# Kernel optimization log

Measured on AMD Instinct MI355X. Metric: run time of the kernel, lower is better.

Reference implementation:

```python
import jax, jax.numpy as jnp
import numpy as np

B, N, T, N_IN = 4, 40, 64, 4
N_EMB, N_HID = 32, 64
EPS = 1e-05


def _spatial_rels(n):
    # fully-connected directed edges without self-loops (NRI convention)
    offdiag = np.ones((n, n)) - np.eye(n)
    recv_idx, send_idx = np.where(offdiag)[0], np.where(offdiag)[1]
    eye = np.eye(n, dtype=np.float32)
    return eye[recv_idx], eye[send_idx]  # [n*(n-1), n] each


def _temporal_rels(t):
    # all t*t ordered pairs (including self), one-hot
    eye = np.eye(t, dtype=np.float32)
    recv = np.repeat(np.arange(t), t)
    send = np.tile(np.arange(t), t)
    return eye[recv], eye[send]  # [t*t, t] each


def setup_inputs() -> dict:
    key = jax.random.key(0)
    ks = jax.random.split(key, 8)
    rel_rec, rel_send = _spatial_rels(N)
    rel_rec_t, rel_send_t = _temporal_rels(T)
    s_emb = 1.0 / np.sqrt(N_IN)
    s_lstm = 1.0 / np.sqrt(N_HID)
    s_att = 1.0 / np.sqrt(2 * N_HID)
    return {
        "inputs": jax.random.normal(ks[0], (B, N, T, N_IN), dtype=jnp.float32),
        "rel_rec": jnp.asarray(rel_rec),
        "rel_send": jnp.asarray(rel_send),
        "rel_rec_t": jnp.asarray(rel_rec_t),
        "rel_send_t": jnp.asarray(rel_send_t),
        "W_emb": jax.random.uniform(ks[1], (N_EMB, N_IN), jnp.float32, -s_emb, s_emb),
        "b_emb": jnp.zeros((N_EMB,), jnp.float32),
        "W_ih": jax.random.uniform(ks[2], (4 * N_HID, N_EMB), jnp.float32, -s_lstm, s_lstm),
        "W_hh": jax.random.uniform(ks[3], (4 * N_HID, N_HID), jnp.float32, -s_lstm, s_lstm),
        "b_ih": jax.random.uniform(ks[4], (4 * N_HID,), jnp.float32, -s_lstm, s_lstm),
        "b_hh": jax.random.uniform(ks[5], (4 * N_HID,), jnp.float32, -s_lstm, s_lstm),
        "W_att": jax.random.uniform(ks[6], (1, 2 * N_HID), jnp.float32, -s_att, s_att),
        "b_att": jnp.zeros((1,), jnp.float32),
    }


def _forward(inputs, rel_rec, rel_send, rel_rec_t, rel_send_t,
             W_emb, b_emb, W_ih, W_hh, b_ih, b_hh, W_att, b_att):
    b, n, t, _ = inputs.shape
    nh = W_hh.shape[1]
    locs = inputs[..., :2]

    # ---- LSTMEncoder: per-timestep embedding + LSTM cell (scan over time) ----
    emb = jnp.einsum("bnti,ei->bnte", inputs, W_emb) + b_emb       # [B,N,T,n_emb]
    xs = emb.transpose(2, 0, 1, 3).reshape(t, b * n, -1)            # [T,BN,n_emb]

    def step(carry, x):
        h, c = carry
        gates = x @ W_ih.T + b_ih + h @ W_hh.T + b_hh               # [BN,4H]
        i_g, f_g, g_g, o_g = jnp.split(gates, 4, axis=-1)           # torch gate order i,f,g,o
        i_g = jax.nn.sigmoid(i_g)
        f_g = jax.nn.sigmoid(f_g)
        g_g = jnp.tanh(g_g)
        o_g = jax.nn.sigmoid(o_g)
        c = f_g * c + i_g * g_g
        h = o_g * jnp.tanh(c)
        return (h, c), h

    h0 = jnp.zeros((b * n, nh), inputs.dtype)
    _, hs_t = jax.lax.scan(step, (h0, h0), xs)                      # [T,BN,H]
    hs = hs_t.transpose(1, 0, 2).reshape(b, n, t, nh)               # [B,N,T,H]

    # ---- SoftAttention over timesteps ----
    hsf = hs.reshape(b * n, t, nh)                                  # [BN,T,H]
    senders = jnp.einsum("kt,mth->mkh", rel_send_t, hsf)            # [BN,T*T,H]
    receivers = jnp.einsum("kt,mth->mkh", rel_rec_t, hsf)
    edges = jnp.concatenate([senders, receivers], axis=-1)          # [BN,T*T,2H]
    scores = jnp.einsum("mkf,of->mko", edges, W_att)[..., 0] + b_att[0]  # [BN,T*T]
    # adj = rel_send_t^T @ diag(scores) @ rel_rec_t (done without diag_embed)
    adj_s = jnp.einsum("ki,mk,kj->mij", rel_send_t, scores, rel_rec_t)   # [BN,T,T]
    adj_sn = jax.nn.softmax(adj_s, axis=-1)
    cs = jnp.einsum("mij,mjh->mih", adj_sn, hsf).reshape(b, n, t, nh)    # [B,N,T,H]

    # ---- HardwiredAttention over atoms ----
    locs_re = locs.reshape(b, n, -1)                                 # [B,N,T*2]
    snd = jnp.einsum("en,bnf->bef", rel_send, locs_re).reshape(b, -1, t, 2)
    rcv = jnp.einsum("en,bnf->bef", rel_rec, locs_re).reshape(b, -1, t, 2)
    dist = jnp.sqrt(((snd - rcv) ** 2).sum(-1))                      # [B,E,T]
    w = (1.0 / (dist + EPS)).transpose(0, 2, 1)                      # [B,T,E]
    adj_h = jnp.einsum("ei,bte,ej->btij", rel_send, w, rel_rec)      # [B,T,N,N]
    ch = jnp.einsum("btij,btjh->btih", adj_h, hs.transpose(0, 2, 1, 3))
    ch = ch.transpose(0, 2, 1, 3)                                    # [B,N,T,H]

    c_out = jnp.tanh(jnp.concatenate([cs[:, :, -1, :], ch.sum(2)], axis=-1))  # [B,N,2H]
    return c_out


def reference(inputs, rel_rec, rel_send, rel_rec_t, rel_send_t,
              W_emb, b_emb, W_ih, W_hh, b_ih, b_hh, W_att, b_att):
    return _forward(inputs, rel_rec, rel_send, rel_rec_t, rel_send_t,
                    W_emb, b_emb, W_ih, W_hh, b_ih, b_hh, W_att, b_att)
```

## Files before the change

kernel.cpp:

```cpp
#include <hip/hip_runtime.h>
#include <math.h>

#define BB   4
#define NN   40
#define TT   64
#define NIN  4
#define NEMB 32
#define NHID 64
#define NG   256
#define EPSW 1e-5f

__device__ __forceinline__ float fast_sigmoid(float x) {
    return __fdividef(1.0f, 1.0f + __expf(-x));
}
__device__ __forceinline__ float fast_tanh(float x) {
    return __fdividef(2.0f, 1.0f + __expf(-2.0f * x)) - 1.0f;
}
__device__ __forceinline__ float lanebcast(float v, int l) {
    return __int_as_float(__builtin_amdgcn_readlane(__float_as_int(v), l));
}

__global__ __launch_bounds__(256, 1)
void k_lstm(const float* __restrict__ inputs,
            const float* __restrict__ W_emb,
            const float* __restrict__ b_emb,
            const float* __restrict__ W_ih,
            const float* __restrict__ W_hh,
            const float* __restrict__ b_ih,
            const float* __restrict__ b_hh,
            const float* __restrict__ W_att,
            float* __restrict__ out,
            float* __restrict__ hs_g)
{
    __shared__ __align__(16) float s_x[TT * NIN];
    __shared__ __align__(16) float s_act[2][NG];
    __shared__ __align__(16) float s_hs[TT * (NHID + 1)];
    __shared__ __align__(16) float s_war[NHID];
    __shared__ __align__(16) float s_p[TT];

    const int m   = blockIdx.x;
    const int tid = threadIdx.x;
    const int g   = tid;
    const int j   = tid & 63;
    const int gtype = g >> 6;

    s_x[tid] = inputs[m * (TT * NIN) + tid];
    if (tid < NHID) s_war[tid] = W_att[NHID + tid];

    float wcx = 0.f, wcy = 0.f, wcz = 0.f, wcw = 0.f;
    float bc  = b_ih[g] + b_hh[g];
    {
        const float4* wih4  = (const float4*)(W_ih + g * NEMB);
        const float4* wemb4 = (const float4*)W_emb;
        #pragma unroll
        for (int e4 = 0; e4 < NEMB / 4; ++e4) {
            float4 wv = wih4[e4];
            float4 m0 = wemb4[4 * e4 + 0];
            float4 m1 = wemb4[4 * e4 + 1];
            float4 m2 = wemb4[4 * e4 + 2];
            float4 m3 = wemb4[4 * e4 + 3];
            wcx += wv.x * m0.x + wv.y * m1.x + wv.z * m2.x + wv.w * m3.x;
            wcy += wv.x * m0.y + wv.y * m1.y + wv.z * m2.y + wv.w * m3.y;
            wcz += wv.x * m0.z + wv.y * m1.z + wv.z * m2.z + wv.w * m3.z;
            wcw += wv.x * m0.w + wv.y * m1.w + wv.z * m2.w + wv.w * m3.w;
            bc  += wv.x * b_emb[4 * e4 + 0] + wv.y * b_emb[4 * e4 + 1]
                 + wv.z * b_emb[4 * e4 + 2] + wv.w * b_emb[4 * e4 + 3];
        }
    }

    const float4* q4 = (const float4*)(W_hh + g * NHID);
    float4 w0 = q4[0],  w1 = q4[1],  w2 = q4[2],  w3 = q4[3];
    float4 w4 = q4[4],  w5 = q4[5],  w6 = q4[6],  w7 = q4[7];
    float4 w8 = q4[8],  w9 = q4[9],  wA = q4[10], wB = q4[11];
    float4 wC = q4[12], wD = q4[13], wE = q4[14], wF = q4[15];
    #define PIN4(W) asm volatile("" : "+v"(W.x), "+v"(W.y), "+v"(W.z), "+v"(W.w))
    PIN4(w0); PIN4(w1); PIN4(w2); PIN4(w3);
    PIN4(w4); PIN4(w5); PIN4(w6); PIN4(w7);
    PIN4(w8); PIN4(w9); PIN4(wA); PIN4(wB);
    PIN4(wC); PIN4(wD); PIN4(wE); PIN4(wF);
    #undef PIN4

    __syncthreads();

    float c = 0.0f, h = 0.0f;
    #pragma unroll 1
    for (int t = 0; t < TT; ++t) {
        const int p = t & 1;
        const float4 x = ((const float4*)s_x)[t];

        float v0 = bc, v1 = 0.f, v2 = 0.f, v3 = 0.f;
        #define DOT4(W, K) {                                  \
            v0 += lanebcast(h, 4*(K)+0) * W.x;                \
            v1 += lanebcast(h, 4*(K)+1) * W.y;                \
            v2 += lanebcast(h, 4*(K)+2) * W.z;                \
            v3 += lanebcast(h, 4*(K)+3) * W.w; }
        DOT4(w0, 0)  DOT4(w1, 1)  DOT4(w2, 2)  DOT4(w3, 3)
        DOT4(w4, 4)  DOT4(w5, 5)  DOT4(w6, 6)  DOT4(w7, 7)
        DOT4(w8, 8)  DOT4(w9, 9)  DOT4(wA, 10) DOT4(wB, 11)
        DOT4(wC, 12) DOT4(wD, 13) DOT4(wE, 14) DOT4(wF, 15)
        #undef DOT4
        const float vx = x.x * wcx + x.y * wcy + x.z * wcz + x.w * wcw;
        const float v  = ((v0 + v1) + (v2 + v3)) + vx;

        const float a = (gtype == 2) ? fast_tanh(v) : fast_sigmoid(v);
        s_act[p][g] = a;
        __syncthreads();

        const float ig = s_act[p][j];
        const float fg = s_act[p][NHID + j];
        const float gg = s_act[p][2 * NHID + j];
        const float og = s_act[p][3 * NHID + j];
        c = fg * c + ig * gg;
        h = og * fast_tanh(c);
        if (gtype == 0) s_hs[t * (NHID + 1) + j] = h;
    }
    __syncthreads();

    #pragma unroll
    for (int idx = tid; idx < TT * NHID; idx += 256) {
        const int t = idx >> 6, hh = idx & 63;
        hs_g[m * (TT * NHID) + idx] = s_hs[t * (NHID + 1) + hh];
    }

    if (tid < TT) {
        const int t = tid;
        float r = 0.0f;
        #pragma unroll
        for (int k = 0; k < NHID; ++k)
            r += s_hs[t * (NHID + 1) + k] * s_war[k];
        float mx = r;
        #pragma unroll
        for (int off = 32; off >= 1; off >>= 1)
            mx = fmaxf(mx, __shfl_xor(mx, off));
        const float e = __expf(r - mx);
        float s = e;
        #pragma unroll
        for (int off = 32; off >= 1; off >>= 1)
            s += __shfl_xor(s, off);
        s_p[t] = __fdividef(e, s);
    }
    __syncthreads();

    if (tid < NHID) {
        float acc = 0.0f;
        #pragma unroll
        for (int t = 0; t < TT; ++t)
            acc += s_p[t] * s_hs[t * (NHID + 1) + tid];
        out[m * (2 * NHID) + tid] = fast_tanh(acc);
    }
}

__global__ __launch_bounds__(256)
void k_spatial(const float* __restrict__ inputs,
               const float* __restrict__ hs_g,
               float* __restrict__ out)
{
    __shared__ float s_w[TT * NN];
    __shared__ float s_part[4 * NHID];

    const int bi  = blockIdx.x;
    const int b   = bi / NN;
    const int i   = bi - b * NN;
    const int tid = threadIdx.x;

    for (int idx = tid; idx < TT * NN; idx += 256) {
        const int t = idx / NN;
        const int j = idx - t * NN;
        const float* pi = inputs + ((b * NN + i) * TT + t) * NIN;
        const float* pj = inputs + ((b * NN + j) * TT + t) * NIN;
        const float dx = pi[0] - pj[0];
        const float dy = pi[1] - pj[1];
        const float d  = sqrtf(dx * dx + dy * dy);
        s_w[idx] = (j == i) ? 0.0f : __fdividef(1.0f, d + EPSW);
    }
    __syncthreads();

    const int h = tid & 63;
    const int q = tid >> 6;

    const float* base = hs_g + (size_t)b * NN * TT * NHID + h;
    float a0 = 0.f, a1 = 0.f, a2 = 0.f, a3 = 0.f;
    for (int t = q * 16; t < q * 16 + 16; ++t) {
        const float* hp = base + t * NHID;
        const float* wp = s_w + t * NN;
        #pragma unroll
        for (int j = 0; j < NN; j += 4) {
            a0 += wp[j + 0] * hp[(size_t)(j + 0) * TT * NHID];
            a1 += wp[j + 1] * hp[(size_t)(j + 1) * TT * NHID];
            a2 += wp[j + 2] * hp[(size_t)(j + 2) * TT * NHID];
            a3 += wp[j + 3] * hp[(size_t)(j + 3) * TT * NHID];
        }
    }
    s_part[q * NHID + h] = (a0 + a1) + (a2 + a3);
    __syncthreads();

    if (tid < NHID) {
        const float s = s_part[tid] + s_part[NHID + tid] +
                        s_part[2 * NHID + tid] + s_part[3 * NHID + tid];
        out[bi * (2 * NHID) + NHID + tid] = fast_tanh(s);
    }
}

extern "C" void kernel_launch(void* const* d_in, const int* in_sizes, int n_in,
                              void* d_out, int out_size, void* d_ws, size_t ws_size,
                              hipStream_t stream) {
    const float* inputs = (const float*)d_in[0];
    const float* W_emb  = (const float*)d_in[5];
    const float* b_emb  = (const float*)d_in[6];
    const float* W_ih   = (const float*)d_in[7];
    const float* W_hh   = (const float*)d_in[8];
    const float* b_ih   = (const float*)d_in[9];
    const float* b_hh   = (const float*)d_in[10];
    const float* W_att  = (const float*)d_in[11];

    float* outp = (float*)d_out;
    float* hs_g = (float*)d_ws;

    hipLaunchKernelGGL(k_lstm, dim3(BB * NN), dim3(256), 0, stream,
                       inputs, W_emb, b_emb, W_ih, W_hh, b_ih, b_hh, W_att,
                       outp, hs_g);
    hipLaunchKernelGGL(k_spatial, dim3(BB * NN), dim3(256), 0, stream,
                       inputs, hs_g, outp);
}
```

Measured before the change: 135.2 us.

## Run LSTM recurrence in a single wavefront per sequence, removing per-step barriers

The LSTM kernel now uses one 64-lane wavefront per sequence, and each lane computes all four gates for its hidden unit. The per-timestep LDS exchange of gate activations and the __syncthreads barrier are removed, and inputs are broadcast across lanes with readlane instead of going through shared memory. The cost is four times the serial FMA work per lane and 256 weight registers per lane, which risks register spilling and lower throughput per step.

```diff
diff --git a/kernel.cpp b/kernel.cpp
--- a/kernel.cpp
+++ b/kernel.cpp
@@ -7,7 +7,6 @@
 #define NIN  4
 #define NEMB 32
 #define NHID 64
-#define NG   256
 #define EPSW 1e-5f
 
 __device__ __forceinline__ float fast_sigmoid(float x) {
@@ -20,7 +19,7 @@
     return __int_as_float(__builtin_amdgcn_readlane(__float_as_int(v), l));
 }
 
-__global__ __launch_bounds__(256, 1)
+__global__ __launch_bounds__(64, 1)
 void k_lstm(const float* __restrict__ inputs,
             const float* __restrict__ W_emb,
             const float* __restrict__ b_emb,
@@ -32,98 +31,101 @@
             float* __restrict__ out,
             float* __restrict__ hs_g)
 {
-    __shared__ __align__(16) float s_x[TT * NIN];
-    __shared__ __align__(16) float s_act[2][NG];
     __shared__ __align__(16) float s_hs[TT * (NHID + 1)];
     __shared__ __align__(16) float s_war[NHID];
     __shared__ __align__(16) float s_p[TT];
 
-    const int m   = blockIdx.x;
-    const int tid = threadIdx.x;
-    const int g   = tid;
-    const int j   = tid & 63;
-    const int gtype = g >> 6;
-
-    s_x[tid] = inputs[m * (TT * NIN) + tid];
-    if (tid < NHID) s_war[tid] = W_att[NHID + tid];
-
-    float wcx = 0.f, wcy = 0.f, wcz = 0.f, wcw = 0.f;
-    float bc  = b_ih[g] + b_hh[g];
+    const int m = blockIdx.x;
+    const int j = threadIdx.x;
+
+    s_war[j] = W_att[NHID + j];
+
+    const float4 xl = ((const float4*)(inputs + m * (TT * NIN)))[j];
+
+    #define FOLD(PFX, ROW)                                                   \
+        float PFX##0 = 0.f, PFX##1 = 0.f, PFX##2 = 0.f, PFX##3 = 0.f;        \
+        float PFX##b = b_ih[ROW] + b_hh[ROW];                                \
+        {                                                                    \
+            const float4* wih4 = (const float4*)(W_ih + (ROW) * NEMB);       \
+            _Pragma("unroll")                                                \
+            for (int e4 = 0; e4 < NEMB / 4; ++e4) {                          \
+                float4 wv = wih4[e4];                                        \
+                const float4* wm = ((const float4*)W_emb) + 4 * e4;          \
+                PFX##0 += wv.x*wm[0].x + wv.y*wm[1].x + wv.z*wm[2].x + wv.w*wm[3].x; \
+                PFX##1 += wv.x*wm[0].y + wv.y*wm[1].y + wv.z*wm[2].y + wv.w*wm[3].y; \
+                PFX##2 += wv.x*wm[0].z + wv.y*wm[1].z + wv.z*wm[2].z + wv.w*wm[3].z; \
+                PFX##3 += wv.x*wm[0].w + wv.y*wm[1].w + wv.z*wm[2].w + wv.w*wm[3].w; \
+                PFX##b += wv.x*b_emb[4*e4+0] + wv.y*b_emb[4*e4+1]            \
+                        + wv.z*b_emb[4*e4+2] + wv.w*b_emb[4*e4+3];           \
+            }                                                                \
+        }
+    FOLD(wcI, j)
+    FOLD(wcF, NHID + j)
+    FOLD(wcG, 2 * NHID + j)
+    FOLD(wcO, 3 * NHID + j)
+    #undef FOLD
+
+    float4 wI[16], wF[16], wG[16], wO[16];
     {
-        const float4* wih4  = (const float4*)(W_ih + g * NEMB);
-        const float4* wemb4 = (const float4*)W_emb;
-        #pragma unroll
-        for (int e4 = 0; e4 < NEMB / 4; ++e4) {
-            float4 wv = wih4[e4];
-            float4 m0 = wemb4[4 * e4 + 0];
-            float4 m1 = wemb4[4 * e4 + 1];
-            float4 m2 = wemb4[4 * e4 + 2];
-            float4 m3 = wemb4[4 * e4 + 3];
-            wcx += wv.x * m0.x + wv.y * m1.x + wv.z * m2.x + wv.w * m3.x;
-            wcy += wv.x * m0.y + wv.y * m1.y + wv.z * m2.y + wv.w * m3.y;
-            wcz += wv.x * m0.z + wv.y * m1.z + wv.z * m2.z + wv.w * m3.z;
-            wcw += wv.x * m0.w + wv.y * m1.w + wv.z * m2.w + wv.w * m3.w;
-            bc  += wv.x * b_emb[4 * e4 + 0] + wv.y * b_emb[4 * e4 + 1]
-                 + wv.z * b_emb[4 * e4 + 2] + wv.w * b_emb[4 * e4 + 3];
-        }
-    }
-
-    const float4* q4 = (const float4*)(W_hh + g * NHID);
-    float4 w0 = q4[0],  w1 = q4[1],  w2 = q4[2],  w3 = q4[3];
-    float4 w4 = q4[4],  w5 = q4[5],  w6 = q4[6],  w7 = q4[7];
-    float4 w8 = q4[8],  w9 = q4[9],  wA = q4[10], wB = q4[11];
-    float4 wC = q4[12], wD = q4[13], wE = q4[14], wF = q4[15];
-    #define PIN4(W) asm volatile("" : "+v"(W.x), "+v"(W.y), "+v"(W.z), "+v"(W.w))
-    PIN4(w0); PIN4(w1); PIN4(w2); PIN4(w3);
-    PIN4(w4); PIN4(w5); PIN4(w6); PIN4(w7);
-    PIN4(w8); PIN4(w9); PIN4(wA); PIN4(wB);
-    PIN4(wC); PIN4(wD); PIN4(wE); PIN4(wF);
-    #undef PIN4
-
-    __syncthreads();
+        const float4* pI = (const float4*)(W_hh + (size_t)(j) * NHID);
+        const float4* pF = (const float4*)(W_hh + (size_t)(NHID + j) * NHID);
+        const float4* pG = (const float4*)(W_hh + (size_t)(2 * NHID + j) * NHID);
+        const float4* pO = (const float4*)(W_hh + (size_t)(3 * NHID + j) * NHID);
+        #pragma unroll
+        for (int k = 0; k < 16; ++k) {
+            wI[k] = pI[k]; wF[k] = pF[k]; wG[k] = pG[k]; wO[k] = pO[k];
+        }
+    }
 
     float c = 0.0f, h = 0.0f;
     #pragma unroll 1
     for (int t = 0; t < TT; ++t) {
-        const int p = t & 1;
-        const float4 x = ((const float4*)s_x)[t];
-
-        float v0 = bc, v1 = 0.f, v2 = 0.f, v3 = 0.f;
-        #define DOT4(W, K) {                                  \
-            v0 += lanebcast(h, 4*(K)+0) * W.x;                \
-            v1 += lanebcast(h, 4*(K)+1) * W.y;                \
-            v2 += lanebcast(h, 4*(K)+2) * W.z;                \
-            v3 += lanebcast(h, 4*(K)+3) * W.w; }
-        DOT4(w0, 0)  DOT4(w1, 1)  DOT4(w2, 2)  DOT4(w3, 3)
-        DOT4(w4, 4)  DOT4(w5, 5)  DOT4(w6, 6)  DOT4(w7, 7)
-        DOT4(w8, 8)  DOT4(w9, 9)  DOT4(wA, 10) DOT4(wB, 11)
-        DOT4(wC, 12) DOT4(wD, 13) DOT4(wE, 14) DOT4(wF, 15)
-        #undef DOT4
-        const float vx = x.x * wcx + x.y * wcy + x.z * wcz + x.w * wcw;
-        const float v  = ((v0 + v1) + (v2 + v3)) + vx;
-
-        const float a = (gtype == 2) ? fast_tanh(v) : fast_sigmoid(v);
-        s_act[p][g] = a;
-        __syncthreads();
-
-        const float ig = s_act[p][j];
-        const float fg = s_act[p][NHID + j];
-        const float gg = s_act[p][2 * NHID + j];
-        const float og = s_act[p][3 * NHID + j];
+        const float xb0 = lanebcast(xl.x, t);
+        const float xb1 = lanebcast(xl.y, t);
+        const float xb2 = lanebcast(xl.z, t);
+        const float xb3 = lanebcast(xl.w, t);
+
+        float aI0 = wcIb + xb0 * wcI0 + xb2 * wcI2;
+        float aI1 = xb1 * wcI1 + xb3 * wcI3;
+        float aF0 = wcFb + xb0 * wcF0 + xb2 * wcF2;
+        float aF1 = xb1 * wcF1 + xb3 * wcF3;
+        float aG0 = wcGb + xb0 * wcG0 + xb2 * wcG2;
+        float aG1 = xb1 * wcG1 + xb3 * wcG3;
+        float aO0 = wcOb + xb0 * wcO0 + xb2 * wcO2;
+        float aO1 = xb1 * wcO1 + xb3 * wcO3;
+
+        #pragma unroll
+        for (int k = 0; k < 16; ++k) {
+            const float h0 = lanebcast(h, 4 * k + 0);
+            const float h1 = lanebcast(h, 4 * k + 1);
+            const float h2 = lanebcast(h, 4 * k + 2);
+            const float h3 = lanebcast(h, 4 * k + 3);
+            aI0 += h0 * wI[k].x; aI1 += h1 * wI[k].y;
+            aI0 += h2 * wI[k].z; aI1 += h3 * wI[k].w;
+            aF0 += h0 * wF[k].x; aF1 += h1 * wF[k].y;
+            aF0 += h2 * wF[k].z; aF1 += h3 * wF[k].w;
+            aG0 += h0 * wG[k].x; aG1 += h1 * wG[k].y;
+            aG0 += h2 * wG[k].z; aG1 += h3 * wG[k].w;
+            aO0 += h0 * wO[k].x; aO1 += h1 * wO[k].y;
+            aO0 += h2 * wO[k].z; aO1 += h3 * wO[k].w;
+        }
+
+        const float ig = fast_sigmoid(aI0 + aI1);
+        const float fg = fast_sigmoid(aF0 + aF1);
+        const float gg = fast_tanh(aG0 + aG1);
+        const float og = fast_sigmoid(aO0 + aO1);
         c = fg * c + ig * gg;
         h = og * fast_tanh(c);
-        if (gtype == 0) s_hs[t * (NHID + 1) + j] = h;
-    }
-    __syncthreads();
-
-    #pragma unroll
-    for (int idx = tid; idx < TT * NHID; idx += 256) {
-        const int t = idx >> 6, hh = idx & 63;
-        hs_g[m * (TT * NHID) + idx] = s_hs[t * (NHID + 1) + hh];
-    }
-
-    if (tid < TT) {
-        const int t = tid;
+        s_hs[t * (NHID + 1) + j] = h;
+    }
+    __syncthreads();
+
+    #pragma unroll 1
+    for (int t = 0; t < TT; ++t)
+        hs_g[m * (TT * NHID) + t * NHID + j] = s_hs[t * (NHID + 1) + j];
+
+    {
+        const int t = j;
         float r = 0.0f;
         #pragma unroll
         for (int k = 0; k < NHID; ++k)
@@ -141,12 +143,12 @@
     }
     __syncthreads();
 
-    if (tid < NHID) {
+    {
         float acc = 0.0f;
         #pragma unroll
         for (int t = 0; t < TT; ++t)
-            acc += s_p[t] * s_hs[t * (NHID + 1) + tid];
-        out[m * (2 * NHID) + tid] = fast_tanh(acc);
+            acc += s_p[t] * s_hs[t * (NHID + 1) + j];
+        out[m * (2 * NHID) + j] = fast_tanh(acc);
     }
 }
 
@@ -216,7 +218,7 @@
     float* outp = (float*)d_out;
     float* hs_g = (float*)d_ws;
 
-    hipLaunchKernelGGL(k_lstm, dim3(BB * NN), dim3(256), 0, stream,
+    hipLaunchKernelGGL(k_lstm, dim3(BB * NN), dim3(64), 0, stream,
                        inputs, W_emb, b_emb, W_ih, W_hh, b_ih, b_hh, W_att,
                        outp, hs_g);
     hipLaunchKernelGGL(k_spatial, dim3(BB * NN), dim3(256), 0, stream,
```

Result: slower. 158.4 us (+17.1%).
